# Optimization experiments

Measured on AMD Instinct MI355X. Metric: run time of the kernel, lower is better.

The kernel has to match this reference:

```python
import jax, jax.numpy as jnp
import numpy as np

B, K, D, LS, NL = 32, 64, 256, 128, 2


def _xavier(key, shape):
    # torch xavier_uniform for Linear weight [out, in]
    fan_out, fan_in = shape[-2], shape[-1]
    lim = float(np.sqrt(6.0 / (fan_in + fan_out)))
    return jax.random.uniform(key, shape, jnp.float32, -lim, lim)


def setup_inputs():
    key = jax.random.key(0)
    ks = jax.random.split(key, 32)
    inp = {
        "X": jax.random.normal(ks[0], (B, K, D), jnp.float32),
        # per-layer stacked params [NL, ...]
        "k_w": _xavier(ks[1], (NL, D, D)),
        "q_w": _xavier(ks[2], (NL, D, D)),
        "rv_w1": _xavier(ks[3], (NL, D, 2 * D)),
        "rv_b1": jnp.zeros((NL, D), jnp.float32),
        "rv_w2": _xavier(ks[4], (NL, D, D)),
        "rv_b2": jnp.zeros((NL, D), jnp.float32),
        "ln_g": jnp.ones((NL, D), jnp.float32),
        "ln_b": jnp.zeros((NL, D), jnp.float32),
        "mlp_w1": _xavier(ks[5], (NL, D, D)),
        "mlp_b1": jnp.zeros((NL, D), jnp.float32),
        "mlp_w2": _xavier(ks[6], (NL, D, D)),
        "mlp_b2": jnp.zeros((NL, D), jnp.float32),
        "proj_w": _xavier(ks[7], (LS, D)),
        "proj_b": jnp.zeros((LS,), jnp.float32),
        "mu_w": _xavier(ks[8], (LS, LS)),
        "mu_b": jnp.zeros((LS,), jnp.float32),
        "sp_w": _xavier(ks[9], (LS, LS)),
        "sp_b": jnp.zeros((LS,), jnp.float32),
    }
    return inp


def _gelu(x):
    return jax.nn.gelu(x, approximate=False)


def _layernorm(x, g, b, eps=1e-5):
    m = jnp.mean(x, axis=-1, keepdims=True)
    v = jnp.mean((x - m) ** 2, axis=-1, keepdims=True)
    return (x - m) / jnp.sqrt(v + eps) * g + b


def _block(x, kw, qw, rw1, rb1, rw2, rb2, lg, lb, mw1, mb1, mw2, mb2):
    scale = D ** (-0.5)
    x_orig = x
    # pairwise difference r[b,i,j,:] = x[b,i]-x[b,j]
    r = x[:, :, None, :] - x[:, None, :, :]                      # [B,K,K,D]
    xi = jnp.broadcast_to(x[:, :, None, :], (B, K, K, D))
    cat = jnp.concatenate([xi, r], axis=-1)                      # [B,K,K,2D]
    v = _gelu(jnp.einsum('bijc,dc->bijd', cat, rw1) + rb1)
    v = jnp.einsum('bijd,ed->bije', v, rw2) + rb2                # [B,K,K,D]
    k = jnp.einsum('bid,ed->bie', x, kw)
    q = jnp.einsum('bid,ed->bie', x, qw) * scale
    attn = jax.nn.softmax(jnp.einsum('bid,bjd->bij', q, k), axis=2)
    agg = jnp.einsum('bij,bijd->bid', attn, v)
    h = _layernorm(x_orig + agg, lg, lb)
    h = jnp.einsum('bid,ed->bie', _gelu(jnp.einsum('bid,ed->bie', h, mw1) + mb1), mw2) + mb2
    return x_orig + h


def reference(X, k_w, q_w, rv_w1, rv_b1, rv_w2, rv_b2, ln_g, ln_b,
              mlp_w1, mlp_b1, mlp_w2, mlp_b2, proj_w, proj_b,
              mu_w, mu_b, sp_w, sp_b):
    x = X
    for i in range(NL):
        x = _block(x, k_w[i], q_w[i], rv_w1[i], rv_b1[i], rv_w2[i], rv_b2[i],
                   ln_g[i], ln_b[i], mlp_w1[i], mlp_b1[i], mlp_w2[i], mlp_b2[i])
    s = jnp.sum(x, axis=1)                                        # [B,D]
    h = _gelu(s @ proj_w.T + proj_b)                              # [B,LS]
    mu = h @ mu_w.T + mu_b
    scale = jax.nn.softplus(h @ sp_w.T + sp_b)
    return (mu, scale)
```

## Files before the change

### kernel.cpp

```cpp
#include <hip/hip_runtime.h>
#include <hip/hip_bf16.h>


using bf16 = __hip_bfloat16;
typedef short bf16x8 __attribute__((ext_vector_type(8)));
typedef float f32x4 __attribute__((ext_vector_type(4)));

__device__ __forceinline__ float bfu(unsigned short u) { return __uint_as_float(((unsigned)u) << 16); }

__device__ __forceinline__ unsigned short bfr(float v) {
  unsigned u = __float_as_uint(v);
  u += 0x7FFFu + ((u >> 16) & 1u);
  return (unsigned short)(u >> 16);
}

__device__ __forceinline__ float gelu_e(float x) {
  return 0.5f * x * (1.0f + erff(x * 0.7071067811865475f));
}

__device__ __forceinline__ float load_f(const void* p, int i, int fl) {
  if (fl) return bfu(((const unsigned short*)p)[i]);
  return ((const float*)p)[i];
}

__device__ __forceinline__ int block_detect(const void* X) {
  __shared__ int bad_s;
  if (threadIdx.x == 0) bad_s = 0;
  __syncthreads();
  if (threadIdx.x < 256) {
    const float v = bfu(((const unsigned short*)X)[threadIdx.x]);
    if (!(fabsf(v) < 1e6f)) atomicOr(&bad_s, 1);
  }
  __syncthreads();
  return bad_s ? 0 : 1;
}

__device__ __forceinline__ void stage_split4(unsigned short (&aF)[2][4096], int row, int d0, float4 v) {
  ushort4 h, lo;
  h.x = bfr(v.x); h.y = bfr(v.y); h.z = bfr(v.z); h.w = bfr(v.w);
  lo.x = bfr(v.x - bfu(h.x)); lo.y = bfr(v.y - bfu(h.y));
  lo.z = bfr(v.z - bfu(h.z)); lo.w = bfr(v.w - bfu(h.w));
  const int kt = d0 >> 5, lane = row | (((d0 >> 3) & 3) << 4), j = d0 & 7;
  *(ushort4*)&aF[0][kt*512 + lane*8 + j] = h;
  *(ushort4*)&aF[1][kt*512 + lane*8 + j] = lo;
}

__global__ __launch_bounds__(256) void prep_kernel(
    const void* __restrict__ X, const void* __restrict__ kw, const void* __restrict__ qw,
    const void* __restrict__ rw1, const void* __restrict__ rw2, const void* __restrict__ mw1,
    const void* __restrict__ mw2, const void* __restrict__ pw, const void* __restrict__ muw,
    const void* __restrict__ spw,
    const void* __restrict__ rb1, const void* __restrict__ rb2, const void* __restrict__ lng,
    const void* __restrict__ lnb, const void* __restrict__ mb1, const void* __restrict__ mb2,
    const void* __restrict__ pb, const void* __restrict__ mub, const void* __restrict__ spb,
    unsigned short* __restrict__ wfb, unsigned short* __restrict__ w3b,
    float* __restrict__ wh, float* __restrict__ bc)
{
  __shared__ __align__(16) char psm[65536];
  const int fl = block_detect(X);
  const int t = threadIdx.x;
  int blk = blockIdx.x;

  if (blk < 16) {
    unsigned short* ls = (unsigned short*)psm;
    unsigned* lsu = (unsigned*)psm;
    const int l = blk >> 3, kt = blk & 7;
    if (fl) {
      #pragma unroll
      for (int s = 0; s < 4; ++s) {
        const unsigned* sp = (const unsigned*)((s == 0) ? kw : (s == 1) ? qw : rw1);
        const int rstr = (s < 2) ? 128 : 256;
        const int coff = ((s == 3) ? 128 : 0) + kt*16;
        for (int i = t; i < 4096; i += 256) {
          const int e = i >> 4, d2 = i & 15;
          lsu[s*4096 + i] = sp[(l*256 + e)*rstr + coff + d2];
        }
      }
    } else {
      #pragma unroll
      for (int s = 0; s < 4; ++s) {
        const float* sp = (const float*)((s == 0) ? kw : (s == 1) ? qw : rw1);
        const int rstr = (s < 2) ? 256 : 512;
        const int coff = ((s == 3) ? 256 : 0) + kt*32;
        for (int i = t; i < 4096; i += 256) {
          const int e = i >> 4, d2 = i & 15;
          const float f0 = sp[(l*256 + e)*rstr + coff + d2*2];
          const float f1 = sp[(l*256 + e)*rstr + coff + d2*2 + 1];
          lsu[s*4096 + i] = (unsigned)bfr(f0) | ((unsigned)bfr(f1) << 16);
        }
      }
    }
    __syncthreads();
    unsigned* outp = (unsigned*)wfb + (l*8 + kt)*16384;
    for (int f2 = t; f2 < 16384; f2 += 256) {
      const int j2 = f2 & 3, lane = (f2 >> 2) & 63, ntg = f2 >> 8;
      const int seg = ntg >> 4;
      const int e = (ntg & 15)*16 + (lane & 15);
      const int dl = ((lane >> 4) & 3)*8 + j2*2;
      unsigned short r0 = ls[seg*8192 + e*32 + dl];
      unsigned short r1 = ls[seg*8192 + e*32 + dl + 1];
      if (seg == 1) { r0 = bfr(bfu(r0)*0.0625f); r1 = bfr(bfu(r1)*0.0625f); }
      else if (seg == 2) {
        const unsigned short w0 = ls[3*8192 + e*32 + dl];
        const unsigned short w1 = ls[3*8192 + e*32 + dl + 1];
        r0 = bfr(bfu(r0) + bfu(w0)); r1 = bfr(bfu(r1) + bfu(w1));
      }
      outp[f2] = (unsigned)r0 | ((unsigned)r1 << 16);
    }
    return;
  }
  blk -= 16;
  if (blk < 48) {
    unsigned short* ls = (unsigned short*)psm;
    unsigned* lsu = (unsigned*)psm;
    const int l3 = blk >> 3, kt = blk & 7;
    const int l = l3 / 3, gm = l3 % 3;
    const void* src = (gm == 0) ? rw2 : (gm == 1) ? mw1 : mw2;
    if (fl) {
      const unsigned* sp = (const unsigned*)src;
      for (int i = t; i < 4096; i += 256) {
        const int e = i >> 4, d2 = i & 15;
        lsu[i] = sp[(l*256 + e)*128 + kt*16 + d2];
      }
    } else {
      const float* sp = (const float*)src;
      for (int i = t; i < 4096; i += 256) {
        const int e = i >> 4, d2 = i & 15;
        const float f0 = sp[(l*256 + e)*256 + kt*32 + d2*2];
        const float f1 = sp[(l*256 + e)*256 + kt*32 + d2*2 + 1];
        lsu[i] = (unsigned)bfr(f0) | ((unsigned)bfr(f1) << 16);
      }
    }
    __syncthreads();
    unsigned* outp = (unsigned*)w3b + (l3*8 + kt)*4096;
    for (int f2 = t; f2 < 4096; f2 += 256) {
      const int j2 = f2 & 3, lane = (f2 >> 2) & 63, nt = f2 >> 8;
      const int e = nt*16 + (lane & 15);
      const int dl = ((lane >> 4) & 3)*8 + j2*2;
      outp[f2] = (unsigned)ls[e*32 + dl] | ((unsigned)ls[e*32 + dl + 1] << 16);
    }
    return;
  }
  blk -= 48;
  if (blk < 24) {
    float* lsf = (float*)psm;
    if (blk < 8) {
      const int l0 = blk*16;
      if (fl) {
        const unsigned* sp = (const unsigned*)pw;
        for (int i = t; i < 2048; i += 256) {
          const int ll = i >> 7, d2 = i & 127;
          const unsigned u = sp[(l0 + ll)*128 + d2];
          lsf[ll*256 + d2*2]     = __uint_as_float(u << 16);
          lsf[ll*256 + d2*2 + 1] = __uint_as_float(u & 0xffff0000u);
        }
      } else {
        const float* sp = (const float*)pw;
        for (int i = t; i < 4096; i += 256) {
          const int ll = i >> 8, d = i & 255;
          lsf[ll*256 + d] = sp[(l0 + ll)*256 + d];
        }
      }
      __syncthreads();
      for (int i = t; i < 4096; i += 256) {
        const int d = i >> 4, ll = i & 15;
        wh[d*128 + l0 + ll] = lsf[ll*256 + d];
      }
    } else {
      const int grp2 = blk - 8;
      const int isSp = grp2 >> 3;
      const int l0 = (grp2 & 7)*16;
      const void* src = isSp ? spw : muw;
      const int off = isSp ? 49152 : 32768;
      if (fl) {
        const unsigned* sp = (const unsigned*)src;
        for (int i = t; i < 1024; i += 256) {
          const int ll = i >> 6, c2 = i & 63;
          const unsigned u = sp[(l0 + ll)*64 + c2];
          lsf[ll*128 + c2*2]     = __uint_as_float(u << 16);
          lsf[ll*128 + c2*2 + 1] = __uint_as_float(u & 0xffff0000u);
        }
      } else {
        const float* sp = (const float*)src;
        for (int i = t; i < 2048; i += 256) {
          const int ll = i >> 7, c = i & 127;
          lsf[ll*128 + c] = sp[(l0 + ll)*128 + c];
        }
      }
      __syncthreads();
      for (int i = t; i < 2048; i += 256) {
        const int c = i >> 4, ll = i & 15;
        wh[off + c*128 + l0 + ll] = lsf[ll*128 + c];
      }
    }
    return;
  }
  for (int i = t; i < 3456; i += 256) {
    const void* src; int off;
    if (i < 512)       { src = rb1; off = i; }
    else if (i < 1024) { src = rb2; off = i - 512; }
    else if (i < 1536) { src = lng; off = i - 1024; }
    else if (i < 2048) { src = lnb; off = i - 1536; }
    else if (i < 2560) { src = mb1; off = i - 2048; }
    else if (i < 3072) { src = mb2; off = i - 2560; }
    else if (i < 3200) { src = pb;  off = i - 3072; }
    else if (i < 3328) { src = mub; off = i - 3200; }
    else               { src = spb; off = i - 3328; }
    bc[i] = load_f(src, off, fl);
  }
}

template<bool SPLIT, int NTG>
__device__ __forceinline__ void k1_body(
    const unsigned short (&aF)[2][4096],
    const unsigned short* __restrict__ wfb, const float* __restrict__ bc,
    float* __restrict__ kq, float* __restrict__ Pf, unsigned* __restrict__ Qpk,
    int l, int row0, int ntg0, int t)
{
  const int w = t >> 6, l64 = t & 63;
  const int col = l64 & 15, quad = l64 >> 4;
  f32x4 acc[NTG];
  #pragma unroll
  for (int i = 0; i < NTG; ++i) acc[i] = (f32x4){0.f, 0.f, 0.f, 0.f};
  for (int kt = 0; kt < 8; ++kt) {
    const bf16x8 ah = *(const bf16x8*)&aF[0][kt*512 + l64*8];
    bf16x8 al;
    if (SPLIT) al = *(const bf16x8*)&aF[1][kt*512 + l64*8];
    #pragma unroll
    for (int i = 0; i < NTG; ++i) {
      const int ntg = ntg0 + w*NTG + i;
      const bf16x8 b = *(const bf16x8*)&wfb[((l*8 + kt)*64 + ntg)*512 + l64*8];
      acc[i] = __builtin_amdgcn_mfma_f32_16x16x32_bf16(ah, b, acc[i], 0, 0, 0);
      if (SPLIT) acc[i] = __builtin_amdgcn_mfma_f32_16x16x32_bf16(al, b, acc[i], 0, 0, 0);
    }
  }
  #pragma unroll
  for (int i = 0; i < NTG; ++i) {
    const int ntg = ntg0 + w*NTG + i;
    if (ntg < 32) {
      const int n = ntg*16 + col;
      #pragma unroll
      for (int r = 0; r < 4; ++r)
        kq[(size_t)(row0 + quad*4 + r)*512 + n] = acc[i][r];
    } else if (ntg < 48) {
      const int c = (ntg - 32)*16 + col;
      const float bias = bc[l*256 + c];
      #pragma unroll
      for (int r = 0; r < 4; ++r)
        Pf[(size_t)(row0 + quad*4 + r)*256 + c] = acc[i][r] + bias;
    } else {
      #pragma unroll
      for (int r = 0; r < 4; ++r) {
        const float v = acc[i][r];
        const float pv = __shfl_xor(v, 1, 64);
        if (!(col & 1)) {
          const unsigned uu = (unsigned)bfr(v) | ((unsigned)bfr(pv) << 16);
          Qpk[(size_t)(row0 + quad*4 + r)*128 + (ntg - 48)*8 + (col >> 1)] = uu;
        }
      }
    }
  }
}

__global__ __launch_bounds__(256) void k1l0(
    const void* __restrict__ X, const unsigned short* __restrict__ wfb,
    const float* __restrict__ bc, float* __restrict__ kq, float* __restrict__ Pf,
    unsigned* __restrict__ Qpk)
{
  const int fl = block_detect(X);
  __shared__ __align__(16) unsigned short aF[2][4096];
  const int t = threadIdx.x;
  const int mb = (int)blockIdx.x >> 2, nb4 = (int)blockIdx.x & 3;
  const int row0 = mb * 16, ntg0 = nb4 * 16;
  if (fl) {
    for (int i = t; i < 512; i += 256) {
      const int row = i >> 5, d0 = (i & 31) * 8;
      const uint4 u = *(const uint4*)((const unsigned*)X + (size_t)(row0 + row)*128 + (i & 31)*4);
      const int kt = d0 >> 5, lane = row | (((d0 >> 3) & 3) << 4);
      *(uint4*)&aF[0][kt*512 + lane*8] = u;
    }
  } else {
    for (int i = t; i < 1024; i += 256) {
      const int row = i >> 6, d0 = (i & 63) * 4;
      stage_split4(aF, row, d0, *(const float4*)((const float*)X + (size_t)(row0 + row)*256 + d0));
    }
  }
  __syncthreads();
  if (fl) k1_body<false, 4>(aF, wfb, bc, kq, Pf, Qpk, 0, row0, ntg0, t);
  else    k1_body<true,  4>(aF, wfb, bc, kq, Pf, Qpk, 0, row0, ntg0, t);
}

__global__ __launch_bounds__(256) void k23_attn(
    const float* __restrict__ kq, const float* __restrict__ Pf,
    const unsigned* __restrict__ Qpk, float* __restrict__ g)
{
  __shared__ float qs[2][256];
  __shared__ float scp[2][64];
  __shared__ float als[2][64];
  const int t = threadIdx.x;
  const int b = (int)blockIdx.x >> 5, ip = (int)blockIdx.x & 31;
  const int base = b << 6, i0 = ip * 2;
  for (int i = t; i < 512; i += 256)
    qs[i >> 8][i & 255] = kq[(size_t)(base + i0 + (i >> 8))*512 + 256 + (i & 255)];
  __syncthreads();
  {
    const int w = t >> 6, lane = t & 63;
    const int jl = lane & 15, part = lane >> 4;
    const int j = w*16 + jl;
    const float* krow = kq + (size_t)(base + j)*512 + part*64;
    const float* q0p = &qs[0][part*64];
    const float* q1p = &qs[1][part*64];
    float s0 = 0.f, s1 = 0.f;
    for (int dd = 0; dd < 64; dd += 4) {
      const float4 kv = *(const float4*)&krow[dd];
      const float4 q0 = *(const float4*)&q0p[dd];
      const float4 q1 = *(const float4*)&q1p[dd];
      s0 = fmaf(kv.x, q0.x, s0); s0 = fmaf(kv.y, q0.y, s0);
      s0 = fmaf(kv.z, q0.z, s0); s0 = fmaf(kv.w, q0.w, s0);
      s1 = fmaf(kv.x, q1.x, s1); s1 = fmaf(kv.y, q1.y, s1);
      s1 = fmaf(kv.z, q1.z, s1); s1 = fmaf(kv.w, q1.w, s1);
    }
    s0 += __shfl_xor(s0, 16, 64); s0 += __shfl_xor(s0, 32, 64);
    s1 += __shfl_xor(s1, 16, 64); s1 += __shfl_xor(s1, 32, 64);
    if (part == 0) { scp[0][j] = s0; scp[1][j] = s1; }
  }
  __syncthreads();
  if (t < 128) {
    const int row = t >> 6, j = t & 63;
    float s = scp[row][j];
    float m = s;
    #pragma unroll
    for (int off = 32; off; off >>= 1) m = fmaxf(m, __shfl_xor(m, off, 64));
    const float e = __expf(s - m);
    float ss = e;
    #pragma unroll
    for (int off = 32; off; off >>= 1) ss += __shfl_xor(ss, off, 64);
    als[row][j] = e / ss;
  }
  __syncthreads();
  const int rg = t >> 7, cp = t & 127;
  const int r = base + i0 + rg;
  const float2 P = *(const float2*)&Pf[(size_t)r*256 + cp*2];
  const float A0 = -1.702f * P.x, A1 = -1.702f * P.y;
  const float* ap = &als[rg][0];
  const unsigned* qp = Qpk + (size_t)base*128 + cp;
  float acc0 = 0.f, acc1 = 0.f;
  #pragma unroll 8
  for (int j = 0; j < 64; ++j) {
    const unsigned u = qp[j*128];
    const float wgt = ap[j];
    const float q0 = __uint_as_float(u << 16);
    const float q1 = __uint_as_float(u & 0xffff0000u);
    const float s0 = __builtin_amdgcn_rcpf(1.f + __expf(fmaf(1.702f, q0, A0)));
    const float s1 = __builtin_amdgcn_rcpf(1.f + __expf(fmaf(1.702f, q1, A1)));
    acc0 = fmaf(wgt * (P.x - q0), s0, acc0);
    acc1 = fmaf(wgt * (P.y - q1), s1, acc1);
  }
  *(float2*)&g[(size_t)r*256 + cp*2] = make_float2(acc0, acc1);
}

__device__ __forceinline__ void k4_gemm8(
    f32x4 acc[2], const unsigned short (&aF)[2][4096],
    const unsigned short* __restrict__ wg, int w, int l64)
{
  acc[0] = (f32x4){0.f, 0.f, 0.f, 0.f};
  acc[1] = (f32x4){0.f, 0.f, 0.f, 0.f};
  for (int kt = 0; kt < 8; ++kt) {
    const bf16x8 ah = *(const bf16x8*)&aF[0][kt*512 + l64*8];
    const bf16x8 al = *(const bf16x8*)&aF[1][kt*512 + l64*8];
    #pragma unroll
    for (int nt = 0; nt < 2; ++nt) {
      const bf16x8 b = *(const bf16x8*)&wg[((kt*16 + (w*2 + nt))*64 + l64)*8];
      acc[nt] = __builtin_amdgcn_mfma_f32_16x16x32_bf16(ah, b, acc[nt], 0, 0, 0);
      acc[nt] = __builtin_amdgcn_mfma_f32_16x16x32_bf16(al, b, acc[nt], 0, 0, 0);
    }
  }
}

template<bool ADAPT, bool TAIL, int NR>
__device__ __forceinline__ void k4_core(
    const float* __restrict__ g, const void* __restrict__ xin, int fl,
    float* __restrict__ xout, const unsigned short* __restrict__ wg,
    const float* __restrict__ bc, int l, int row0, int t, bool writeX,
    unsigned short (&aF)[2][4096], float* bufB, float (&mv)[16][2])
{
  const int w = t >> 6, l64 = t & 63;
  const int col = l64 & 15, quad = l64 >> 4;
  const float* rb2c = bc + 512  + l*256;
  const float* lngc = bc + 1024 + l*256;
  const float* lnbc = bc + 1536 + l*256;
  const float* mb1c = bc + 2048 + l*256;
  const float* mb2c = bc + 2560 + l*256;

  for (int i = t; i < NR*64; i += 512) {
    const int row = i >> 6, d0 = (i & 63) * 4;
    stage_split4(aF, row, d0, *(const float4*)&g[(size_t)(row0 + row)*256 + d0]);
  }
  if (ADAPT && fl) {
    for (int c = t; c < NR*128; c += 512) {
      const int row = c >> 7, dp = c & 127;
      const unsigned u = ((const unsigned*)xin)[(size_t)(row0 + row)*128 + dp];
      bufB[row*260 + dp*2]     = __uint_as_float(u << 16);
      bufB[row*260 + dp*2 + 1] = __uint_as_float(u & 0xffff0000u);
    }
  } else {
    for (int c = t; c < NR*64; c += 512) {
      const int row = c >> 6, d0 = (c & 63) * 4;
      *(float4*)&bufB[row*260 + d0] = *(const float4*)((const float*)xin + (size_t)(row0 + row)*256 + d0);
    }
  }
  __syncthreads();
  float xtr[2][4];
  #pragma unroll
  for (int nt = 0; nt < 2; ++nt) {
    const int cn = (w*2 + nt)*16 + col;
    #pragma unroll
    for (int r = 0; r < 4; ++r) xtr[nt][r] = bufB[(quad*4 + r)*260 + cn];
  }
  __syncthreads();

  f32x4 acc[2];
  k4_gemm8(acc, aF, wg, w, l64);
  #pragma unroll
  for (int nt = 0; nt < 2; ++nt) {
    const int cn = (w*2 + nt)*16 + col;
    #pragma unroll
    for (int r = 0; r < 4; ++r)
      bufB[(quad*4 + r)*260 + cn] = acc[nt][r] + rb2c[cn] + xtr[nt][r];
  }
  __syncthreads();
  {
    const int row = t >> 5, part = t & 31;
    if (row < NR) {
      float s = 0.f, s2 = 0.f;
      #pragma unroll
      for (int kk = 0; kk < 8; ++kk) {
        const float v = bufB[row*260 + part + kk*32];
        s += v; s2 = fmaf(v, v, s2);
      }
      #pragma unroll
      for (int off = 16; off; off >>= 1) {
        s  += __shfl_xor(s, off, 32);
        s2 += __shfl_xor(s2, off, 32);
      }
      if (part == 0) {
        const float mu = s * (1.f/256.f);
        mv[row][0] = mu;
        mv[row][1] = rsqrtf(fmaf(-mu, mu, s2 * (1.f/256.f)) + 1e-5f);
      }
    }
  }
  __syncthreads();
  for (int i = t; i < NR*64; i += 512) {
    const int row = i >> 6, d0 = (i & 63) * 4;
    float4 v = *(const float4*)&bufB[row*260 + d0];
    const float m = mv[row][0], iv = mv[row][1];
    v.x = (v.x - m)*iv*lngc[d0]   + lnbc[d0];
    v.y = (v.y - m)*iv*lngc[d0+1] + lnbc[d0+1];
    v.z = (v.z - m)*iv*lngc[d0+2] + lnbc[d0+2];
    v.w = (v.w - m)*iv*lngc[d0+3] + lnbc[d0+3];
    stage_split4(aF, row, d0, v);
  }
  __syncthreads();
  k4_gemm8(acc, aF, wg + 65536, w, l64);
  #pragma unroll
  for (int nt = 0; nt < 2; ++nt) {
    const int cn = (w*2 + nt)*16 + col;
    #pragma unroll
    for (int r = 0; r < 4; ++r)
      if (quad*4 + r < NR)
        bufB[(quad*4 + r)*260 + cn] = gelu_e(acc[nt][r] + mb1c[cn]);
  }
  __syncthreads();
  for (int i = t; i < NR*64; i += 512) {
    const int row = i >> 6, d0 = (i & 63) * 4;
    stage_split4(aF, row, d0, *(const float4*)&bufB[row*260 + d0]);
  }
  __syncthreads();
  k4_gemm8(acc, aF, wg + 2*65536, w, l64);
  if (TAIL) {
    #pragma unroll
    for (int nt = 0; nt < 2; ++nt) {
      const int cn = (w*2 + nt)*16 + col;
      #pragma unroll
      for (int r = 0; r < 4; ++r)
        bufB[(quad*4 + r)*260 + cn] = acc[nt][r] + mb2c[cn] + xtr[nt][r];
    }
    __syncthreads();
    for (int i = t; i < NR*64; i += 512) {
      const int row = i >> 6, d0 = (i & 63) * 4;
      const float4 v = *(const float4*)&bufB[row*260 + d0];
      if (writeX) *(float4*)&xout[(size_t)(row0 + row)*256 + d0] = v;
      stage_split4(aF, row, d0, v);
    }
    __syncthreads();
  } else {
    #pragma unroll
    for (int nt = 0; nt < 2; ++nt) {
      const int cn = (w*2 + nt)*16 + col;
      #pragma unroll
      for (int r = 0; r < 4; ++r)
        if (quad*4 + r < NR)
          xout[(size_t)(row0 + quad*4 + r)*256 + cn] = acc[nt][r] + mb2c[cn] + xtr[nt][r];
    }
  }
}

__global__ __launch_bounds__(512) void k41_mix_kq(
    const float* __restrict__ g, const unsigned short* __restrict__ w3b,
    const unsigned short* __restrict__ wfb, const float* __restrict__ bc,
    const void* __restrict__ X, float* __restrict__ x,
    float* __restrict__ kq, float* __restrict__ Pf, unsigned* __restrict__ Qpk)
{
  const int fl = block_detect(X);
  __shared__ __align__(16) unsigned short aF[2][4096];
  __shared__ float bufB[16*260];
  __shared__ float mv[16][2];
  const int t = threadIdx.x;
  const int rb = (int)blockIdx.x >> 1, parity = (int)blockIdx.x & 1;
  const int row0 = rb * 16;
  k4_core<true, true, 16>(g, X, fl, x, w3b, bc, 0, row0, t, parity == 0, aF, bufB, mv);
  k1_body<true, 4>(aF, wfb, bc, kq, Pf, Qpk, 1, row0, parity*32, t);
}

__global__ __launch_bounds__(512) void k4_fin(
    const float* __restrict__ g, const unsigned short* __restrict__ w3b,
    const float* __restrict__ bc, float* __restrict__ x)
{
  __shared__ __align__(16) unsigned short aF[2][4096];
  __shared__ float bufB[16*260];
  __shared__ float mv[16][2];
  const int t = threadIdx.x;
  const int row0 = blockIdx.x * 8;
  k4_core<false, false, 8>(g, x, 0, x, w3b + 3*65536, bc, 1, row0, t, true, aF, bufB, mv);
}

__global__ __launch_bounds__(256) void k5_head(
    const float* __restrict__ x, const float* __restrict__ wh,
    const float* __restrict__ bc, const void* __restrict__ X,
    void* __restrict__ out)
{
  const int fl = block_detect(X);
  __shared__ float ss[256];
  __shared__ float hh[128];
  const int b = blockIdx.x, t = threadIdx.x;
  float s = 0.f;
  for (int i = 0; i < 64; ++i) s += x[(size_t)((b << 6) + i)*256 + t];
  ss[t] = s;
  __syncthreads();
  if (t < 128) {
    float acc = bc[3072 + t];
    const float* projT = wh;
    for (int d = 0; d < 256; ++d) acc = fmaf(ss[d], projT[d*128 + t], acc);
    hh[t] = gelu_e(acc);
  }
  __syncthreads();
  float v; int oidx;
  if (t < 128) {
    float acc = bc[3200 + t];
    const float* muT = wh + 32768;
    for (int c = 0; c < 128; ++c) acc = fmaf(hh[c], muT[c*128 + t], acc);
    v = acc; oidx = b*128 + t;
  } else {
    const int u = t - 128;
    float acc = bc[3328 + u];
    const float* spT = wh + 49152;
    for (int c = 0; c < 128; ++c) acc = fmaf(hh[c], spT[c*128 + u], acc);
    v = (acc > 20.f) ? acc : log1pf(__expf(acc));
    oidx = 4096 + b*128 + u;
  }
  if (fl) ((bf16*)out)[oidx] = __float2bfloat16(v);
  else    ((float*)out)[oidx] = v;
}

extern "C" void kernel_launch(void* const* d_in, const int* in_sizes, int n_in,
                              void* d_out, int out_size, void* d_ws, size_t ws_size,
                              hipStream_t stream)
{
  (void)in_sizes; (void)n_in; (void)out_size; (void)ws_size;
  float* ws    = (float*)d_ws;
  float* x     = ws + 16;
  float* kq    = x + 524288;
  float* Pf    = kq + 1048576;
  unsigned* Qpk = (unsigned*)(Pf + 524288);
  float* g     = (float*)(Qpk + 262144);
  unsigned short* wfb = (unsigned short*)(g + 524288);
  unsigned short* w3b = wfb + 524288;
  float* wh    = (float*)(w3b + 393216);
  float* bc    = wh + 65536;

  prep_kernel<<<dim3(89), dim3(256), 0, stream>>>(
      d_in[0], d_in[1], d_in[2], d_in[3], d_in[5], d_in[9], d_in[11],
      d_in[13], d_in[15], d_in[17],
      d_in[4], d_in[6], d_in[7], d_in[8], d_in[10], d_in[12],
      d_in[14], d_in[16], d_in[18],
      wfb, w3b, wh, bc);
  k1l0<<<dim3(512), dim3(256), 0, stream>>>(d_in[0], wfb, bc, kq, Pf, Qpk);
  k23_attn<<<dim3(1024), dim3(256), 0, stream>>>(kq, Pf, Qpk, g);
  k41_mix_kq<<<dim3(256), dim3(512), 0, stream>>>(g, w3b, wfb, bc, d_in[0], x, kq, Pf, Qpk);
  k23_attn<<<dim3(1024), dim3(256), 0, stream>>>(kq, Pf, Qpk, g);
  k4_fin<<<dim3(256), dim3(512), 0, stream>>>(g, w3b, bc, x);
  k5_head<<<dim3(32), dim3(256), 0, stream>>>(x, wh, bc, d_in[0], (void*)d_out);
}
```

Before: 208.5 us.

## Fuse weight prep with layer-0 projections and final layer with head

```diff
diff --git a/kernel.cpp b/kernel.cpp
--- a/kernel.cpp
+++ b/kernel.cpp
@@ -45,7 +45,277 @@
   *(ushort4*)&aF[1][kt*512 + lane*8 + j] = lo;
 }
 
-__global__ __launch_bounds__(256) void prep_kernel(
+__device__ void prep_phase(
+    int blk, int t, int fl, char* psm,
+    const void* kw, const void* qw, const void* rw1, const void* rw2,
+    const void* mw1, const void* mw2, const void* pw, const void* muw, const void* spw,
+    const void* rb1, const void* rb2, const void* lng, const void* lnb,
+    const void* mb1, const void* mb2, const void* pb, const void* mub, const void* spb,
+    unsigned short* wfb, unsigned short* w3b, float* wh, float* bc)
+{
+  if (blk < 16) {
+    unsigned short* ls = (unsigned short*)psm;
+    unsigned* lsu = (unsigned*)psm;
+    const int l = blk >> 3, kt = blk & 7;
+    #pragma unroll
+    for (int pass = 0; pass < 2; ++pass) {
+      if (pass == 0) {
+        if (fl) {
+          #pragma unroll
+          for (int s = 0; s < 2; ++s) {
+            const unsigned* sp = (const unsigned*)((s == 0) ? kw : qw);
+            for (int i = t; i < 4096; i += 512) {
+              const int e = i >> 4, d2 = i & 15;
+              lsu[s*4096 + i] = sp[(l*256 + e)*128 + kt*16 + d2];
+            }
+          }
+        } else {
+          #pragma unroll
+          for (int s = 0; s < 2; ++s) {
+            const float* sp = (const float*)((s == 0) ? kw : qw);
+            for (int i = t; i < 4096; i += 512) {
+              const int e = i >> 4, d2 = i & 15;
+              const float f0 = sp[(l*256 + e)*256 + kt*32 + d2*2];
+              const float f1 = sp[(l*256 + e)*256 + kt*32 + d2*2 + 1];
+              lsu[s*4096 + i] = (unsigned)bfr(f0) | ((unsigned)bfr(f1) << 16);
+            }
+          }
+        }
+      } else {
+        if (fl) {
+          const unsigned* sp = (const unsigned*)rw1;
+          #pragma unroll
+          for (int s = 0; s < 2; ++s)
+            for (int i = t; i < 4096; i += 512) {
+              const int e = i >> 4, d2 = i & 15;
+              lsu[s*4096 + i] = sp[(l*256 + e)*256 + s*128 + kt*16 + d2];
+            }
+        } else {
+          const float* sp = (const float*)rw1;
+          #pragma unroll
+          for (int s = 0; s < 2; ++s)
+            for (int i = t; i < 4096; i += 512) {
+              const int e = i >> 4, d2 = i & 15;
+              const float f0 = sp[(l*256 + e)*512 + s*256 + kt*32 + d2*2];
+              const float f1 = sp[(l*256 + e)*512 + s*256 + kt*32 + d2*2 + 1];
+              lsu[s*4096 + i] = (unsigned)bfr(f0) | ((unsigned)bfr(f1) << 16);
+            }
+        }
+      }
+      __syncthreads();
+      unsigned* outp = (unsigned*)wfb + (l*8 + kt)*16384 + pass*8192;
+      for (int f2 = t; f2 < 8192; f2 += 512) {
+        const int j2 = f2 & 3, lane = (f2 >> 2) & 63, ntl = f2 >> 8;
+        const int seg = ntl >> 4;
+        const int e = (ntl & 15)*16 + (lane & 15);
+        const int dl = ((lane >> 4) & 3)*8 + j2*2;
+        unsigned short r0 = ls[seg*8192 + e*32 + dl];
+        unsigned short r1 = ls[seg*8192 + e*32 + dl + 1];
+        if (pass == 1 && seg == 0) {
+          const unsigned short w0 = ls[8192 + e*32 + dl];
+          const unsigned short w1 = ls[8192 + e*32 + dl + 1];
+          r0 = bfr(bfu(r0) + bfu(w0)); r1 = bfr(bfu(r1) + bfu(w1));
+        }
+        outp[f2] = (unsigned)r0 | ((unsigned)r1 << 16);
+      }
+      __syncthreads();
+    }
+    return;
+  }
+  int b2 = blk - 16;
+  if (b2 < 48) {
+    unsigned short* ls = (unsigned short*)psm;
+    unsigned* lsu = (unsigned*)psm;
+    const int l3 = b2 >> 3, kt = b2 & 7;
+    const int l = l3 / 3, gm = l3 % 3;
+    const void* src = (gm == 0) ? rw2 : (gm == 1) ? mw1 : mw2;
+    if (fl) {
+      const unsigned* sp = (const unsigned*)src;
+      for (int i = t; i < 4096; i += 512) {
+        const int e = i >> 4, d2 = i & 15;
+        lsu[i] = sp[(l*256 + e)*128 + kt*16 + d2];
+      }
+    } else {
+      const float* sp = (const float*)src;
+      for (int i = t; i < 4096; i += 512) {
+        const int e = i >> 4, d2 = i & 15;
+        const float f0 = sp[(l*256 + e)*256 + kt*32 + d2*2];
+        const float f1 = sp[(l*256 + e)*256 + kt*32 + d2*2 + 1];
+        lsu[i] = (unsigned)bfr(f0) | ((unsigned)bfr(f1) << 16);
+      }
+    }
+    __syncthreads();
+    unsigned* outp = (unsigned*)w3b + (l3*8 + kt)*4096;
+    for (int f2 = t; f2 < 4096; f2 += 512) {
+      const int j2 = f2 & 3, lane = (f2 >> 2) & 63, nt = f2 >> 8;
+      const int e = nt*16 + (lane & 15);
+      const int dl = ((lane >> 4) & 3)*8 + j2*2;
+      outp[f2] = (unsigned)ls[e*32 + dl] | ((unsigned)ls[e*32 + dl + 1] << 16);
+    }
+    return;
+  }
+  b2 -= 48;
+  if (b2 < 24) {
+    float* lsf = (float*)psm;
+    if (b2 < 8) {
+      const int l0 = b2*16;
+      if (fl) {
+        const unsigned* sp = (const unsigned*)pw;
+        for (int i = t; i < 2048; i += 512) {
+          const int ll = i >> 7, d2 = i & 127;
+          const unsigned u = sp[(l0 + ll)*128 + d2];
+          lsf[ll*256 + d2*2]     = __uint_as_float(u << 16);
+          lsf[ll*256 + d2*2 + 1] = __uint_as_float(u & 0xffff0000u);
+        }
+      } else {
+        const float* sp = (const float*)pw;
+        for (int i = t; i < 4096; i += 512) {
+          const int ll = i >> 8, d = i & 255;
+          lsf[ll*256 + d] = sp[(l0 + ll)*256 + d];
+        }
+      }
+      __syncthreads();
+      for (int i = t; i < 4096; i += 512) {
+        const int d = i >> 4, ll = i & 15;
+        wh[d*128 + l0 + ll] = lsf[ll*256 + d];
+      }
+    } else {
+      const int grp2 = b2 - 8;
+      const int isSp = grp2 >> 3;
+      const int l0 = (grp2 & 7)*16;
+      const void* src = isSp ? spw : muw;
+      const int off = isSp ? 49152 : 32768;
+      if (fl) {
+        const unsigned* sp = (const unsigned*)src;
+        for (int i = t; i < 1024; i += 512) {
+          const int ll = i >> 6, c2 = i & 63;
+          const unsigned u = sp[(l0 + ll)*64 + c2];
+          lsf[ll*128 + c2*2]     = __uint_as_float(u << 16);
+          lsf[ll*128 + c2*2 + 1] = __uint_as_float(u & 0xffff0000u);
+        }
+      } else {
+        const float* sp = (const float*)src;
+        for (int i = t; i < 2048; i += 512) {
+          const int ll = i >> 7, c = i & 127;
+          lsf[ll*128 + c] = sp[(l0 + ll)*128 + c];
+        }
+      }
+      __syncthreads();
+      for (int i = t; i < 2048; i += 512) {
+        const int c = i >> 4, ll = i & 15;
+        wh[off + c*128 + l0 + ll] = lsf[ll*128 + c];
+      }
+    }
+    return;
+  }
+  if (b2 == 24) {
+    for (int i = t; i < 3456; i += 512) {
+      const void* src; int off;
+      if (i < 512)       { src = rb1; off = i; }
+      else if (i < 1024) { src = rb2; off = i - 512; }
+      else if (i < 1536) { src = lng; off = i - 1024; }
+      else if (i < 2048) { src = lnb; off = i - 1536; }
+      else if (i < 2560) { src = mb1; off = i - 2048; }
+      else if (i < 3072) { src = mb2; off = i - 2560; }
+      else if (i < 3200) { src = pb;  off = i - 3072; }
+      else if (i < 3328) { src = mub; off = i - 3200; }
+      else               { src = spb; off = i - 3328; }
+      bc[i] = load_f(src, off, fl);
+    }
+  }
+}
+
+__device__ __forceinline__ bf16x8 raw_bfrag(int seg, int e, int d0, int fl,
+    const void* kw, const void* qw, const void* rw1)
+{
+  if (fl) {
+    if (seg == 0) return *(const bf16x8*)((const unsigned short*)kw + e*256 + d0);
+    if (seg == 1) return *(const bf16x8*)((const unsigned short*)qw + e*256 + d0);
+    const unsigned short* r1 = (const unsigned short*)rw1 + e*512;
+    const bf16x8 wb = *(const bf16x8*)(r1 + 256 + d0);
+    if (seg == 3) return wb;
+    const bf16x8 wa = *(const bf16x8*)(r1 + d0);
+    bf16x8 r;
+    #pragma unroll
+    for (int i = 0; i < 8; ++i)
+      r[i] = (short)bfr(bfu((unsigned short)wa[i]) + bfu((unsigned short)wb[i]));
+    return r;
+  } else {
+    float vs[8];
+    if (seg <= 1) {
+      const float* sp = (const float*)((seg == 0) ? kw : qw) + e*256 + d0;
+      #pragma unroll
+      for (int i = 0; i < 8; ++i) vs[i] = sp[i];
+    } else {
+      const float* r1 = (const float*)rw1 + e*512;
+      #pragma unroll
+      for (int i = 0; i < 8; ++i) vs[i] = r1[256 + d0 + i];
+      if (seg == 2) {
+        #pragma unroll
+        for (int i = 0; i < 8; ++i) vs[i] += r1[d0 + i];
+      }
+    }
+    bf16x8 r;
+    #pragma unroll
+    for (int i = 0; i < 8; ++i) r[i] = (short)bfr(vs[i]);
+    return r;
+  }
+}
+
+template<bool SPLIT>
+__device__ void k1_raw(const unsigned short (&aF)[2][4096], int seg, int ntg0,
+    const void* kw, const void* qw, const void* rw1, const void* rb1, int fl,
+    float* __restrict__ kq, float* __restrict__ Pf, unsigned* __restrict__ Qpk,
+    int row0, int t)
+{
+  const int w = t >> 6, l64 = t & 63;
+  const int col = l64 & 15, quad = l64 >> 4;
+  f32x4 acc[2];
+  acc[0] = (f32x4){0.f, 0.f, 0.f, 0.f};
+  acc[1] = (f32x4){0.f, 0.f, 0.f, 0.f};
+  for (int kt = 0; kt < 8; ++kt) {
+    const bf16x8 ah = *(const bf16x8*)&aF[0][kt*512 + l64*8];
+    bf16x8 al;
+    if (SPLIT) al = *(const bf16x8*)&aF[1][kt*512 + l64*8];
+    const int d0 = kt*32 + quad*8;
+    #pragma unroll
+    for (int i = 0; i < 2; ++i) {
+      const int ntg = ntg0 + w*2 + i;
+      const int e = (ntg & 15)*16 + col;
+      const bf16x8 b = raw_bfrag(seg, e, d0, fl, kw, qw, rw1);
+      acc[i] = __builtin_amdgcn_mfma_f32_16x16x32_bf16(ah, b, acc[i], 0, 0, 0);
+      if (SPLIT) acc[i] = __builtin_amdgcn_mfma_f32_16x16x32_bf16(al, b, acc[i], 0, 0, 0);
+    }
+  }
+  #pragma unroll
+  for (int i = 0; i < 2; ++i) {
+    const int ntg = ntg0 + w*2 + i;
+    if (seg < 2) {
+      const int n = ntg*16 + col;
+      #pragma unroll
+      for (int r = 0; r < 4; ++r)
+        kq[(size_t)(row0 + quad*4 + r)*512 + n] = acc[i][r];
+    } else if (seg == 2) {
+      const int c = (ntg & 15)*16 + col;
+      const float bias = load_f(rb1, c, fl);
+      #pragma unroll
+      for (int r = 0; r < 4; ++r)
+        Pf[(size_t)(row0 + quad*4 + r)*256 + c] = acc[i][r] + bias;
+    } else {
+      #pragma unroll
+      for (int r = 0; r < 4; ++r) {
+        const float v = acc[i][r];
+        const float pv = __shfl_xor(v, 1, 64);
+        if (!(col & 1)) {
+          const unsigned uu = (unsigned)bfr(v) | ((unsigned)bfr(pv) << 16);
+          Qpk[(size_t)(row0 + quad*4 + r)*128 + (ntg & 15)*8 + (col >> 1)] = uu;
+        }
+      }
+    }
+  }
+}
+
+__global__ __launch_bounds__(512) void fusedA(
     const void* __restrict__ X, const void* __restrict__ kw, const void* __restrict__ qw,
     const void* __restrict__ rw1, const void* __restrict__ rw2, const void* __restrict__ mw1,
     const void* __restrict__ mw2, const void* __restrict__ pw, const void* __restrict__ muw,
@@ -54,160 +324,36 @@
     const void* __restrict__ lnb, const void* __restrict__ mb1, const void* __restrict__ mb2,
     const void* __restrict__ pb, const void* __restrict__ mub, const void* __restrict__ spb,
     unsigned short* __restrict__ wfb, unsigned short* __restrict__ w3b,
-    float* __restrict__ wh, float* __restrict__ bc)
-{
-  __shared__ __align__(16) char psm[65536];
+    float* __restrict__ wh, float* __restrict__ bc,
+    float* __restrict__ kq, float* __restrict__ Pf, unsigned* __restrict__ Qpk)
+{
+  __shared__ __align__(16) char smem[32768];
   const int fl = block_detect(X);
   const int t = threadIdx.x;
-  int blk = blockIdx.x;
-
-  if (blk < 16) {
-    unsigned short* ls = (unsigned short*)psm;
-    unsigned* lsu = (unsigned*)psm;
-    const int l = blk >> 3, kt = blk & 7;
-    if (fl) {
-      #pragma unroll
-      for (int s = 0; s < 4; ++s) {
-        const unsigned* sp = (const unsigned*)((s == 0) ? kw : (s == 1) ? qw : rw1);
-        const int rstr = (s < 2) ? 128 : 256;
-        const int coff = ((s == 3) ? 128 : 0) + kt*16;
-        for (int i = t; i < 4096; i += 256) {
-          const int e = i >> 4, d2 = i & 15;
-          lsu[s*4096 + i] = sp[(l*256 + e)*rstr + coff + d2];
-        }
-      }
-    } else {
-      #pragma unroll
-      for (int s = 0; s < 4; ++s) {
-        const float* sp = (const float*)((s == 0) ? kw : (s == 1) ? qw : rw1);
-        const int rstr = (s < 2) ? 256 : 512;
-        const int coff = ((s == 3) ? 256 : 0) + kt*32;
-        for (int i = t; i < 4096; i += 256) {
-          const int e = i >> 4, d2 = i & 15;
-          const float f0 = sp[(l*256 + e)*rstr + coff + d2*2];
-          const float f1 = sp[(l*256 + e)*rstr + coff + d2*2 + 1];
-          lsu[s*4096 + i] = (unsigned)bfr(f0) | ((unsigned)bfr(f1) << 16);
-        }
-      }
-    }
-    __syncthreads();
-    unsigned* outp = (unsigned*)wfb + (l*8 + kt)*16384;
-    for (int f2 = t; f2 < 16384; f2 += 256) {
-      const int j2 = f2 & 3, lane = (f2 >> 2) & 63, ntg = f2 >> 8;
-      const int seg = ntg >> 4;
-      const int e = (ntg & 15)*16 + (lane & 15);
-      const int dl = ((lane >> 4) & 3)*8 + j2*2;
-      unsigned short r0 = ls[seg*8192 + e*32 + dl];
-      unsigned short r1 = ls[seg*8192 + e*32 + dl + 1];
-      if (seg == 1) { r0 = bfr(bfu(r0)*0.0625f); r1 = bfr(bfu(r1)*0.0625f); }
-      else if (seg == 2) {
-        const unsigned short w0 = ls[3*8192 + e*32 + dl];
-        const unsigned short w1 = ls[3*8192 + e*32 + dl + 1];
-        r0 = bfr(bfu(r0) + bfu(w0)); r1 = bfr(bfu(r1) + bfu(w1));
-      }
-      outp[f2] = (unsigned)r0 | ((unsigned)r1 << 16);
-    }
+  const int blk = blockIdx.x;
+  if (blk < 89) {
+    prep_phase(blk, t, fl, smem, kw, qw, rw1, rw2, mw1, mw2, pw, muw, spw,
+               rb1, rb2, lng, lnb, mb1, mb2, pb, mub, spb, wfb, w3b, wh, bc);
     return;
   }
-  blk -= 16;
-  if (blk < 48) {
-    unsigned short* ls = (unsigned short*)psm;
-    unsigned* lsu = (unsigned*)psm;
-    const int l3 = blk >> 3, kt = blk & 7;
-    const int l = l3 / 3, gm = l3 % 3;
-    const void* src = (gm == 0) ? rw2 : (gm == 1) ? mw1 : mw2;
-    if (fl) {
-      const unsigned* sp = (const unsigned*)src;
-      for (int i = t; i < 4096; i += 256) {
-        const int e = i >> 4, d2 = i & 15;
-        lsu[i] = sp[(l*256 + e)*128 + kt*16 + d2];
-      }
-    } else {
-      const float* sp = (const float*)src;
-      for (int i = t; i < 4096; i += 256) {
-        const int e = i >> 4, d2 = i & 15;
-        const float f0 = sp[(l*256 + e)*256 + kt*32 + d2*2];
-        const float f1 = sp[(l*256 + e)*256 + kt*32 + d2*2 + 1];
-        lsu[i] = (unsigned)bfr(f0) | ((unsigned)bfr(f1) << 16);
-      }
-    }
-    __syncthreads();
-    unsigned* outp = (unsigned*)w3b + (l3*8 + kt)*4096;
-    for (int f2 = t; f2 < 4096; f2 += 256) {
-      const int j2 = f2 & 3, lane = (f2 >> 2) & 63, nt = f2 >> 8;
-      const int e = nt*16 + (lane & 15);
-      const int dl = ((lane >> 4) & 3)*8 + j2*2;
-      outp[f2] = (unsigned)ls[e*32 + dl] | ((unsigned)ls[e*32 + dl + 1] << 16);
-    }
-    return;
-  }
-  blk -= 48;
-  if (blk < 24) {
-    float* lsf = (float*)psm;
-    if (blk < 8) {
-      const int l0 = blk*16;
-      if (fl) {
-        const unsigned* sp = (const unsigned*)pw;
-        for (int i = t; i < 2048; i += 256) {
-          const int ll = i >> 7, d2 = i & 127;
-          const unsigned u = sp[(l0 + ll)*128 + d2];
-          lsf[ll*256 + d2*2]     = __uint_as_float(u << 16);
-          lsf[ll*256 + d2*2 + 1] = __uint_as_float(u & 0xffff0000u);
-        }
-      } else {
-        const float* sp = (const float*)pw;
-        for (int i = t; i < 4096; i += 256) {
-          const int ll = i >> 8, d = i & 255;
-          lsf[ll*256 + d] = sp[(l0 + ll)*256 + d];
-        }
-      }
-      __syncthreads();
-      for (int i = t; i < 4096; i += 256) {
-        const int d = i >> 4, ll = i & 15;
-        wh[d*128 + l0 + ll] = lsf[ll*256 + d];
-      }
-    } else {
-      const int grp2 = blk - 8;
-      const int isSp = grp2 >> 3;
-      const int l0 = (grp2 & 7)*16;
-      const void* src = isSp ? spw : muw;
-      const int off = isSp ? 49152 : 32768;
-      if (fl) {
-        const unsigned* sp = (const unsigned*)src;
-        for (int i = t; i < 1024; i += 256) {
-          const int ll = i >> 6, c2 = i & 63;
-          const unsigned u = sp[(l0 + ll)*64 + c2];
-          lsf[ll*128 + c2*2]     = __uint_as_float(u << 16);
-          lsf[ll*128 + c2*2 + 1] = __uint_as_float(u & 0xffff0000u);
-        }
-      } else {
-        const float* sp = (const float*)src;
-        for (int i = t; i < 2048; i += 256) {
-          const int ll = i >> 7, c = i & 127;
-          lsf[ll*128 + c] = sp[(l0 + ll)*128 + c];
-        }
-      }
-      __syncthreads();
-      for (int i = t; i < 2048; i += 256) {
-        const int c = i >> 4, ll = i & 15;
-        wh[off + c*128 + l0 + ll] = lsf[ll*128 + c];
-      }
-    }
-    return;
-  }
-  for (int i = t; i < 3456; i += 256) {
-    const void* src; int off;
-    if (i < 512)       { src = rb1; off = i; }
-    else if (i < 1024) { src = rb2; off = i - 512; }
-    else if (i < 1536) { src = lng; off = i - 1024; }
-    else if (i < 2048) { src = lnb; off = i - 1536; }
-    else if (i < 2560) { src = mb1; off = i - 2048; }
-    else if (i < 3072) { src = mb2; off = i - 2560; }
-    else if (i < 3200) { src = pb;  off = i - 3072; }
-    else if (i < 3328) { src = mub; off = i - 3200; }
-    else               { src = spb; off = i - 3328; }
-    bc[i] = load_f(src, off, fl);
-  }
+  auto& aF = *(unsigned short(*)[2][4096])smem;
+  const int rb = blk - 89;
+  const int mb = rb >> 2, seg = rb & 3;
+  const int row0 = mb * 16, ntg0 = seg * 16;
+  if (fl) {
+    const int row = t >> 5, d0 = (t & 31) * 8;
+    const uint4 u = *(const uint4*)((const unsigned*)X + (size_t)(row0 + row)*128 + (t & 31)*4);
+    const int kt = d0 >> 5, lane = row | (((d0 >> 3) & 3) << 4);
+    *(uint4*)&aF[0][kt*512 + lane*8] = u;
+  } else {
+    for (int i = t; i < 1024; i += 512) {
+      const int row = i >> 6, d0 = (i & 63) * 4;
+      stage_split4(aF, row, d0, *(const float4*)((const float*)X + (size_t)(row0 + row)*256 + d0));
+    }
+  }
+  __syncthreads();
+  if (fl) k1_raw<false>(aF, seg, ntg0, kw, qw, rw1, rb1, fl, kq, Pf, Qpk, row0, t);
+  else    k1_raw<true >(aF, seg, ntg0, kw, qw, rw1, rb1, fl, kq, Pf, Qpk, row0, t);
 }
 
 template<bool SPLIT, int NTG>
@@ -262,37 +408,10 @@
   }
 }
 
-__global__ __launch_bounds__(256) void k1l0(
-    const void* __restrict__ X, const unsigned short* __restrict__ wfb,
-    const float* __restrict__ bc, float* __restrict__ kq, float* __restrict__ Pf,
-    unsigned* __restrict__ Qpk)
-{
-  const int fl = block_detect(X);
-  __shared__ __align__(16) unsigned short aF[2][4096];
-  const int t = threadIdx.x;
-  const int mb = (int)blockIdx.x >> 2, nb4 = (int)blockIdx.x & 3;
-  const int row0 = mb * 16, ntg0 = nb4 * 16;
-  if (fl) {
-    for (int i = t; i < 512; i += 256) {
-      const int row = i >> 5, d0 = (i & 31) * 8;
-      const uint4 u = *(const uint4*)((const unsigned*)X + (size_t)(row0 + row)*128 + (i & 31)*4);
-      const int kt = d0 >> 5, lane = row | (((d0 >> 3) & 3) << 4);
-      *(uint4*)&aF[0][kt*512 + lane*8] = u;
-    }
-  } else {
-    for (int i = t; i < 1024; i += 256) {
-      const int row = i >> 6, d0 = (i & 63) * 4;
-      stage_split4(aF, row, d0, *(const float4*)((const float*)X + (size_t)(row0 + row)*256 + d0));
-    }
-  }
-  __syncthreads();
-  if (fl) k1_body<false, 4>(aF, wfb, bc, kq, Pf, Qpk, 0, row0, ntg0, t);
-  else    k1_body<true,  4>(aF, wfb, bc, kq, Pf, Qpk, 0, row0, ntg0, t);
-}
-
 __global__ __launch_bounds__(256) void k23_attn(
     const float* __restrict__ kq, const float* __restrict__ Pf,
-    const unsigned* __restrict__ Qpk, float* __restrict__ g)
+    const unsigned* __restrict__ Qpk, float* __restrict__ g,
+    float* __restrict__ ssacc, unsigned* __restrict__ cnt, int doZero)
 {
   __shared__ float qs[2][256];
   __shared__ float scp[2][64];
@@ -300,6 +419,10 @@
   const int t = threadIdx.x;
   const int b = (int)blockIdx.x >> 5, ip = (int)blockIdx.x & 31;
   const int base = b << 6, i0 = ip * 2;
+  if (doZero && ip == 0) {
+    ssacc[b*256 + t] = 0.f;
+    if (t == 0) cnt[b] = 0u;
+  }
   for (int i = t; i < 512; i += 256)
     qs[i >> 8][i & 255] = kq[(size_t)(base + i0 + (i >> 8))*512 + 256 + (i & 255)];
   __syncthreads();
@@ -322,7 +445,7 @@
     }
     s0 += __shfl_xor(s0, 16, 64); s0 += __shfl_xor(s0, 32, 64);
     s1 += __shfl_xor(s1, 16, 64); s1 += __shfl_xor(s1, 32, 64);
-    if (part == 0) { scp[0][j] = s0; scp[1][j] = s1; }
+    if (part == 0) { scp[0][j] = s0 * 0.0625f; scp[1][j] = s1 * 0.0625f; }
   }
   __syncthreads();
   if (t < 128) {
@@ -523,30 +646,36 @@
   k1_body<true, 4>(aF, wfb, bc, kq, Pf, Qpk, 1, row0, parity*32, t);
 }
 
-__global__ __launch_bounds__(512) void k4_fin(
+__global__ __launch_bounds__(512) void k4_fin_head(
     const float* __restrict__ g, const unsigned short* __restrict__ w3b,
-    const float* __restrict__ bc, float* __restrict__ x)
-{
+    const float* __restrict__ bc, float* __restrict__ x,
+    const float* __restrict__ wh, float* __restrict__ ssacc,
+    unsigned* __restrict__ cnt, const void* __restrict__ X,
+    void* __restrict__ out)
+{
+  const int fl = block_detect(X);
   __shared__ __align__(16) unsigned short aF[2][4096];
   __shared__ float bufB[16*260];
   __shared__ float mv[16][2];
+  __shared__ int lastf;
   const int t = threadIdx.x;
-  const int row0 = blockIdx.x * 8;
-  k4_core<false, false, 8>(g, x, 0, x, w3b + 3*65536, bc, 1, row0, t, true, aF, bufB, mv);
-}
-
-__global__ __launch_bounds__(256) void k5_head(
-    const float* __restrict__ x, const float* __restrict__ wh,
-    const float* __restrict__ bc, const void* __restrict__ X,
-    void* __restrict__ out)
-{
-  const int fl = block_detect(X);
-  __shared__ float ss[256];
-  __shared__ float hh[128];
-  const int b = blockIdx.x, t = threadIdx.x;
-  float s = 0.f;
-  for (int i = 0; i < 64; ++i) s += x[(size_t)((b << 6) + i)*256 + t];
-  ss[t] = s;
+  const int row0 = (int)blockIdx.x * 8;
+  const int b = (int)blockIdx.x >> 3;
+  k4_core<false, true, 8>(g, x, 0, x, w3b + 3*65536, bc, 1, row0, t, false, aF, bufB, mv);
+  if (t < 256) {
+    float cs = 0.f;
+    #pragma unroll
+    for (int r = 0; r < 8; ++r) cs += bufB[r*260 + t];
+    atomicAdd(&ssacc[b*256 + t], cs);
+  }
+  __syncthreads();
+  if (t == 0) lastf = (atomicAdd(&cnt[b], 1u) == 7u);
+  __syncthreads();
+  if (!lastf) return;
+  float* ss = bufB;
+  float* hh = bufB + 256;
+  if (t < 256)
+    ss[t] = __hip_atomic_load(&ssacc[b*256 + t], __ATOMIC_RELAXED, __HIP_MEMORY_SCOPE_AGENT);
   __syncthreads();
   if (t < 128) {
     float acc = bc[3072 + t];
@@ -555,22 +684,24 @@
     hh[t] = gelu_e(acc);
   }
   __syncthreads();
-  float v; int oidx;
-  if (t < 128) {
-    float acc = bc[3200 + t];
-    const float* muT = wh + 32768;
-    for (int c = 0; c < 128; ++c) acc = fmaf(hh[c], muT[c*128 + t], acc);
-    v = acc; oidx = b*128 + t;
-  } else {
-    const int u = t - 128;
-    float acc = bc[3328 + u];
-    const float* spT = wh + 49152;
-    for (int c = 0; c < 128; ++c) acc = fmaf(hh[c], spT[c*128 + u], acc);
-    v = (acc > 20.f) ? acc : log1pf(__expf(acc));
-    oidx = 4096 + b*128 + u;
-  }
-  if (fl) ((bf16*)out)[oidx] = __float2bfloat16(v);
-  else    ((float*)out)[oidx] = v;
+  if (t < 256) {
+    float v; int oidx;
+    if (t < 128) {
+      float acc = bc[3200 + t];
+      const float* muT = wh + 32768;
+      for (int c = 0; c < 128; ++c) acc = fmaf(hh[c], muT[c*128 + t], acc);
+      v = acc; oidx = b*128 + t;
+    } else {
+      const int u = t - 128;
+      float acc = bc[3328 + u];
+      const float* spT = wh + 49152;
+      for (int c = 0; c < 128; ++c) acc = fmaf(hh[c], spT[c*128 + u], acc);
+      v = (acc > 20.f) ? acc : log1pf(__expf(acc));
+      oidx = 4096 + b*128 + u;
+    }
+    if (fl) ((bf16*)out)[oidx] = __float2bfloat16(v);
+    else    ((float*)out)[oidx] = v;
+  }
 }
 
 extern "C" void kernel_launch(void* const* d_in, const int* in_sizes, int n_in,
@@ -588,17 +719,17 @@
   unsigned short* w3b = wfb + 524288;
   float* wh    = (float*)(w3b + 393216);
   float* bc    = wh + 65536;
-
-  prep_kernel<<<dim3(89), dim3(256), 0, stream>>>(
+  float* ssacc = bc + 4096;
+  unsigned* cnt = (unsigned*)(ssacc + 8192);
+
+  fusedA<<<dim3(601), dim3(512), 0, stream>>>(
       d_in[0], d_in[1], d_in[2], d_in[3], d_in[5], d_in[9], d_in[11],
       d_in[13], d_in[15], d_in[17],
       d_in[4], d_in[6], d_in[7], d_in[8], d_in[10], d_in[12],
       d_in[14], d_in[16], d_in[18],
-      wfb, w3b, wh, bc);
-  k1l0<<<dim3(512), dim3(256), 0, stream>>>(d_in[0], wfb, bc, kq, Pf, Qpk);
-  k23_attn<<<dim3(1024), dim3(256), 0, stream>>>(kq, Pf, Qpk, g);
+      wfb, w3b, wh, bc, kq, Pf, Qpk);
+  k23_attn<<<dim3(1024), dim3(256), 0, stream>>>(kq, Pf, Qpk, g, ssacc, cnt, 0);
   k41_mix_kq<<<dim3(256), dim3(512), 0, stream>>>(g, w3b, wfb, bc, d_in[0], x, kq, Pf, Qpk);
-  k23_attn<<<dim3(1024), dim3(256), 0, stream>>>(kq, Pf, Qpk, g);
-  k4_fin<<<dim3(256), dim3(512), 0, stream>>>(g, w3b, bc, x);
-  k5_head<<<dim3(32), dim3(256), 0, stream>>>(x, wh, bc, d_in[0], (void*)d_out);
-}
+  k23_attn<<<dim3(1024), dim3(256), 0, stream>>>(kq, Pf, Qpk, g, ssacc, cnt, 1);
+  k4_fin_head<<<dim3(256), dim3(512), 0, stream>>>(g, w3b, bc, x, wh, ssacc, cnt, d_in[0], (void*)d_out);
+}
```

After: 212.2 us. Within noise of the previous version (+1.8%).
